# Optimization experiments

Hardware: AMD Instinct MI355X
Metric: run time of the kernel (lower is better)

Reference implementation:

```python
import jax, jax.numpy as jnp
import numpy as np

D_MODEL = 512
N_PAIRS = D_MODEL // 2
B, T = 8, 4096


def setup_inputs() -> dict:
    key = jax.random.key(0)
    ks = jax.random.split(key, 7)
    scale = 1.0 / np.sqrt(D_MODEL)
    return {
        "x_seq": jax.random.normal(ks[0], (B, T, D_MODEL), dtype=jnp.float32),
        "W_angle": jax.random.uniform(ks[1], (D_MODEL, N_PAIRS), jnp.float32, -scale, scale),
        "b_angle": jnp.zeros((N_PAIRS,), jnp.float32),
        "W_decay": jax.random.uniform(ks[2], (D_MODEL, 1), jnp.float32, -scale, scale),
        "b_decay": jnp.full((1,), 1.4, jnp.float32),
        "W_input": jax.random.uniform(ks[3], (D_MODEL, D_MODEL), jnp.float32, -scale, scale),
        "b_input": jax.random.uniform(ks[4], (D_MODEL,), jnp.float32, -scale, scale),
    }


def _givens_ssm(x_seq, W_angle, b_angle, W_decay, b_decay, W_input, b_input):
    Bb, Tt, D = x_seq.shape
    P = D // 2
    angles = jnp.einsum("btd,dp->btp", x_seq, W_angle) + b_angle          # [B,T,P]
    decays = jax.nn.sigmoid(jnp.einsum("btd,dk->btk", x_seq, W_decay) + b_decay)[..., 0]  # [B,T]
    inj = jnp.einsum("btd,de->bte", x_seq, W_input) + b_input              # [B,T,D]
    inj = inj.reshape(Bb, Tt, P, 2)

    # scan over time: h_t = decay_t * Rot(angles_t) h_{t-1} + inj_t, pairwise 2x2 rotations
    def step(h, inp):
        a, d, u = inp  # a:[B,P], d:[B], u:[B,P,2]
        c, s = jnp.cos(a), jnp.sin(a)
        he = c * h[..., 0] - s * h[..., 1]
        ho = s * h[..., 0] + c * h[..., 1]
        h_new = d[:, None, None] * jnp.stack([he, ho], axis=-1) + u
        return h_new, h_new

    h0 = jnp.zeros((Bb, P, 2), x_seq.dtype)
    xs = (jnp.swapaxes(angles, 0, 1), jnp.swapaxes(decays, 0, 1), jnp.swapaxes(inj, 0, 1))
    _, states = jax.lax.scan(step, h0, xs)  # [T,B,P,2]
    return jnp.swapaxes(states, 0, 1).reshape(Bb, Tt, D)


def reference(x_seq, W_angle, b_angle, W_decay, b_decay, W_input, b_input):
    return _givens_ssm(x_seq, W_angle, b_angle, W_decay, b_decay, W_input, b_input)
```

## Files before the change

kernel.cpp:

```cpp
#include <hip/hip_runtime.h>
#include <math.h>

typedef _Float16 half_t;
typedef __attribute__((ext_vector_type(8))) _Float16 half8;
typedef __attribute__((ext_vector_type(2))) _Float16 half2v;
typedef __attribute__((ext_vector_type(4))) float floatx4;

#define BATCH   8
#define SEQ     4096
#define DM      512
#define NP      256
#define M_TOT   32768
#define NTOT    768
#define CHUNKS  128
#define CHUNK_LEN 32

__device__ __forceinline__ void async_load16(const void* g, void* l) {
    __builtin_amdgcn_global_load_lds((const __attribute__((address_space(1))) void*)g,
                                     (__attribute__((address_space(3))) void*)l,
                                     16, 0, 0);
}

__global__ __launch_bounds__(256) void decay_convert(const float* __restrict__ X,
                                                     const float* __restrict__ Wd,
                                                     const float* __restrict__ bd,
                                                     float* __restrict__ dec,
                                                     half_t* __restrict__ Xh) {
    const int wave = threadIdx.x >> 6;
    const int lane = threadIdx.x & 63;
    const int row0 = blockIdx.x * 8 + wave * 2;
    const float4* x0 = (const float4*)(X + (size_t)row0 * DM);
    const float4* x1 = x0 + 128;
    const float4* wd = (const float4*)Wd;
    float4 a0 = x0[2 * lane], a1 = x0[2 * lane + 1];
    float4 b0 = x1[2 * lane], b1 = x1[2 * lane + 1];
    float4 w0 = wd[2 * lane], w1 = wd[2 * lane + 1];
    float s0 = a0.x * w0.x + a0.y * w0.y + a0.z * w0.z + a0.w * w0.w
             + a1.x * w1.x + a1.y * w1.y + a1.z * w1.z + a1.w * w1.w;
    float s1 = b0.x * w0.x + b0.y * w0.y + b0.z * w0.z + b0.w * w0.w
             + b1.x * w1.x + b1.y * w1.y + b1.z * w1.z + b1.w * w1.w;
    half8 h0 = {(half_t)a0.x, (half_t)a0.y, (half_t)a0.z, (half_t)a0.w,
                (half_t)a1.x, (half_t)a1.y, (half_t)a1.z, (half_t)a1.w};
    half8 h1 = {(half_t)b0.x, (half_t)b0.y, (half_t)b0.z, (half_t)b0.w,
                (half_t)b1.x, (half_t)b1.y, (half_t)b1.z, (half_t)b1.w};
    *(half8*)(Xh + (size_t)row0 * DM + lane * 8) = h0;
    *(half8*)(Xh + (size_t)(row0 + 1) * DM + lane * 8) = h1;
#pragma unroll
    for (int off = 32; off > 0; off >>= 1) {
        s0 += __shfl_down(s0, off, 64);
        s1 += __shfl_down(s1, off, 64);
    }
    if (lane == 0) {
        dec[row0]     = 1.0f / (1.0f + __expf(-(s0 + bd[0])));
        dec[row0 + 1] = 1.0f / (1.0f + __expf(-(s1 + bd[0])));
    }
}

__global__ __launch_bounds__(256) void wcat_transpose(const float* __restrict__ Wi,
                                                      const float* __restrict__ Wa,
                                                      half_t* __restrict__ Wt) {
    const int idx = blockIdx.x * 256 + threadIdx.x;
    const int n = idx >> 9;
    const int k = idx & 511;
    float v = (n < DM) ? Wi[(size_t)k * DM + n] : Wa[(size_t)k * NP + (n - DM)];
    Wt[idx] = (half_t)v;
}

__global__ __launch_bounds__(256) void gemm_fused(const half_t* __restrict__ Xh,
                                                  const half_t* __restrict__ Wt,
                                                  const float* __restrict__ bi,
                                                  const float* __restrict__ ba,
                                                  float* __restrict__ out,
                                                  half_t* __restrict__ angles) {
    __shared__ __align__(16) char As[8192];
    __shared__ __align__(16) char Bs[8192];

    const int bm   = blockIdx.x;
    const int bn   = blockIdx.y;
    const int tid  = threadIdx.x;
    const int wave = tid >> 6;
    const int lane = tid & 63;
    const int quad = lane >> 4;
    const int l16  = lane & 15;
    const int wrow = wave >> 1;
    const int wcol = wave & 1;

    floatx4 acc[4][4];
#pragma unroll
    for (int i = 0; i < 4; ++i)
#pragma unroll
        for (int j = 0; j < 4; ++j) acc[i][j] = (floatx4){0.f, 0.f, 0.f, 0.f};

    const int s0 = wave * 128 + lane;
    const int s1 = s0 + 64;
    const int r0 = s0 >> 2, kql0 = (s0 & 3) ^ ((r0 >> 1) & 3);
    const int r1 = s1 >> 2, kql1 = (s1 & 3) ^ ((r1 >> 1) & 3);
    const half_t* gA0 = Xh + (size_t)(bm * 128 + r0) * DM + kql0 * 8;
    const half_t* gA1 = Xh + (size_t)(bm * 128 + r1) * DM + kql1 * 8;
    const half_t* gB0 = Wt + (size_t)(bn * 128 + r0) * DM + kql0 * 8;
    const half_t* gB1 = Wt + (size_t)(bn * 128 + r1) * DM + kql1 * 8;
    char* lA0 = As + wave * 2048;
    char* lA1 = As + wave * 2048 + 1024;
    char* lB0 = Bs + wave * 2048;
    char* lB1 = Bs + wave * 2048 + 1024;

    for (int k0 = 0; k0 < DM; k0 += 32) {
        async_load16(gA0 + k0, lA0);
        async_load16(gA1 + k0, lA1);
        async_load16(gB0 + k0, lB0);
        async_load16(gB1 + k0, lB1);
        __syncthreads();

        half8 af[4], bf[4];
#pragma unroll
        for (int mt = 0; mt < 4; ++mt) {
            const int r = wrow * 64 + mt * 16 + l16;
            af[mt] = *(const half8*)(As + r * 64 + ((quad ^ ((r >> 1) & 3)) << 4));
        }
#pragma unroll
        for (int nt = 0; nt < 4; ++nt) {
            const int r = wcol * 64 + nt * 16 + l16;
            bf[nt] = *(const half8*)(Bs + r * 64 + ((quad ^ ((r >> 1) & 3)) << 4));
        }
#pragma unroll
        for (int mt = 0; mt < 4; ++mt)
#pragma unroll
            for (int nt = 0; nt < 4; ++nt)
                acc[mt][nt] = __builtin_amdgcn_mfma_f32_16x16x32_f16(af[mt], bf[nt],
                                                                     acc[mt][nt], 0, 0, 0);
        __syncthreads();
    }

    const int colbase = bn * 128 + wcol * 64;
#pragma unroll
    for (int nt = 0; nt < 4; ++nt) {
        const int col = colbase + nt * 16 + l16;
        const bool is_inj = col < DM;
        const float bias = is_inj ? bi[col] : ba[col - DM];
#pragma unroll
        for (int mt = 0; mt < 4; ++mt) {
            const int rowb = bm * 128 + wrow * 64 + mt * 16 + quad * 4;
#pragma unroll
            for (int r = 0; r < 4; ++r) {
                const float v = acc[mt][nt][r] + bias;
                const int row = rowb + r;
                if (is_inj) out[(size_t)row * DM + col] = v;
                else        angles[(size_t)row * NP + (col - DM)] = (half_t)v;
            }
        }
    }
}

__global__ __launch_bounds__(256) void scan_sum1(const half_t* __restrict__ angles,
                                                 const float* __restrict__ decays,
                                                 const float* __restrict__ inj,
                                                 float* __restrict__ thetaC,
                                                 float4* __restrict__ hend,
                                                 float* __restrict__ Dprod) {
    const int b   = blockIdx.x >> 6;
    const int sub = threadIdx.x >> 7;
    const int th  = threadIdx.x & 127;
    const int c   = (blockIdx.x & 63) * 2 + sub;
    const int p0  = th * 2;
    const int t0  = c * CHUNK_LEN;

    const half_t* ap = angles + (size_t)(b * SEQ + t0) * NP + p0;
    const float4* up = (const float4*)inj + (size_t)(b * SEQ + t0) * 128 + (p0 >> 1);
    const float*  dp = decays + b * SEQ + t0;

    half2v ab[2][8]; float4 ub[2][8]; float db[2][8];
#pragma unroll
    for (int j = 0; j < 8; ++j) {
        ab[0][j] = *(const half2v*)(ap + (size_t)j * NP);
        ub[0][j] = up[(size_t)j * 128];
        db[0][j] = dp[j];
    }

    float h0a = 0, h1a = 0, h0b = 0, h1b = 0, tha = 0, thb = 0, dc = 1.0f;
#pragma unroll
    for (int g = 0; g < 4; ++g) {
        const int cur = g & 1, nxt = cur ^ 1;
        if (g < 3) {
#pragma unroll
            for (int j = 0; j < 8; ++j) {
                const int t = (g + 1) * 8 + j;
                ab[nxt][j] = *(const half2v*)(ap + (size_t)t * NP);
                ub[nxt][j] = up[(size_t)t * 128];
                db[nxt][j] = dp[t];
            }
        }
#pragma unroll
        for (int j = 0; j < 8; ++j) {
            float a0 = (float)ab[cur][j][0], a1 = (float)ab[cur][j][1];
            float4 u = ub[cur][j];
            float d  = db[cur][j];
            float s0, c0, s1, c1;
            __sincosf(a0, &s0, &c0);
            __sincosf(a1, &s1, &c1);
            float n0a = fmaf(d, c0 * h0a - s0 * h1a, u.x);
            float n1a = fmaf(d, s0 * h0a + c0 * h1a, u.y);
            float n0b = fmaf(d, c1 * h0b - s1 * h1b, u.z);
            float n1b = fmaf(d, s1 * h0b + c1 * h1b, u.w);
            h0a = n0a; h1a = n1a; h0b = n0b; h1b = n1b;
            tha += a0; thb += a1; dc *= d;
        }
    }
    const size_t cbase = (size_t)(b * CHUNKS + c) * NP + p0;
    *(float2*)(thetaC + cbase) = make_float2(tha, thb);
    hend[cbase >> 1] = make_float4(h0a, h1a, h0b, h1b);
    if (th == 0) Dprod[b * CHUNKS + c] = dc;
}

__global__ __launch_bounds__(128) void scan_chunks(const float* __restrict__ thetaC,
                                                   const float4* __restrict__ hend,
                                                   const float* __restrict__ Dprod,
                                                   float4* __restrict__ hentry) {
    const int b  = blockIdx.x;
    const int p0 = threadIdx.x * 2;
    const float2* tp = (const float2*)thetaC + (size_t)b * CHUNKS * 128 + (p0 >> 1);
    const float4* hp = hend + (size_t)b * CHUNKS * 128 + (p0 >> 1);
    float4*       ep = hentry + (size_t)b * CHUNKS * 128 + (p0 >> 1);
    const float*  Dp = Dprod + b * CHUNKS;

    float2 tb[2][4]; float4 hb[2][4]; float Db[2][4];
#pragma unroll
    for (int j = 0; j < 4; ++j) {
        tb[0][j] = tp[(size_t)j * 128];
        hb[0][j] = hp[(size_t)j * 128];
        Db[0][j] = Dp[j];
    }

    float h0a = 0, h1a = 0, h0b = 0, h1b = 0;
#pragma unroll
    for (int g = 0; g < 32; ++g) {
        const int cur = g & 1, nxt = cur ^ 1;
        if (g < 31) {
#pragma unroll
            for (int j = 0; j < 4; ++j) {
                const int c = (g + 1) * 4 + j;
                tb[nxt][j] = tp[(size_t)c * 128];
                hb[nxt][j] = hp[(size_t)c * 128];
                Db[nxt][j] = Dp[c];
            }
        }
#pragma unroll
        for (int j = 0; j < 4; ++j) {
            const int c = g * 4 + j;
            ep[(size_t)c * 128] = make_float4(h0a, h1a, h0b, h1b);
            float2 th2 = tb[cur][j];
            float4 he  = hb[cur][j];
            float D    = Db[cur][j];
            float s0, c0, s1, c1;
            __sincosf(th2.x, &s0, &c0);
            __sincosf(th2.y, &s1, &c1);
            float n0a = fmaf(D, c0 * h0a - s0 * h1a, he.x);
            float n1a = fmaf(D, s0 * h0a + c0 * h1a, he.y);
            float n0b = fmaf(D, c1 * h0b - s1 * h1b, he.z);
            float n1b = fmaf(D, s1 * h0b + c1 * h1b, he.w);
            h0a = n0a; h1a = n1a; h0b = n0b; h1b = n1b;
        }
    }
}

__global__ __launch_bounds__(256) void scan_final(const half_t* __restrict__ angles,
                                                  const float* __restrict__ decays,
                                                  const float4* __restrict__ hentry,
                                                  float* __restrict__ out) {
    const int b   = blockIdx.x >> 6;
    const int sub = threadIdx.x >> 7;
    const int th  = threadIdx.x & 127;
    const int c   = (blockIdx.x & 63) * 2 + sub;
    const int p0  = th * 2;
    const int t0  = c * CHUNK_LEN;

    const half_t* ap = angles + (size_t)(b * SEQ + t0) * NP + p0;
    float4*       op = (float4*)out + (size_t)(b * SEQ + t0) * 128 + (p0 >> 1);
    const float*  dp = decays + b * SEQ + t0;

    float4 v = hentry[(size_t)(b * CHUNKS + c) * 128 + (p0 >> 1)];
    float h0a = v.x, h1a = v.y, h0b = v.z, h1b = v.w;

    half2v ab[2][8]; float4 ub[2][8]; float db[2][8];
#pragma unroll
    for (int j = 0; j < 8; ++j) {
        ab[0][j] = *(const half2v*)(ap + (size_t)j * NP);
        ub[0][j] = op[(size_t)j * 128];
        db[0][j] = dp[j];
    }

#pragma unroll
    for (int g = 0; g < 4; ++g) {
        const int cur = g & 1, nxt = cur ^ 1;
        if (g < 3) {
#pragma unroll
            for (int j = 0; j < 8; ++j) {
                const int t = (g + 1) * 8 + j;
                ab[nxt][j] = *(const half2v*)(ap + (size_t)t * NP);
                ub[nxt][j] = op[(size_t)t * 128];
                db[nxt][j] = dp[t];
            }
        }
#pragma unroll
        for (int j = 0; j < 8; ++j) {
            const int t = g * 8 + j;
            float a0 = (float)ab[cur][j][0], a1 = (float)ab[cur][j][1];
            float4 u = ub[cur][j];
            float d  = db[cur][j];
            float s0, c0, s1, c1;
            __sincosf(a0, &s0, &c0);
            __sincosf(a1, &s1, &c1);
            float n0a = fmaf(d, c0 * h0a - s0 * h1a, u.x);
            float n1a = fmaf(d, s0 * h0a + c0 * h1a, u.y);
            float n0b = fmaf(d, c1 * h0b - s1 * h1b, u.z);
            float n1b = fmaf(d, s1 * h0b + c1 * h1b, u.w);
            h0a = n0a; h1a = n1a; h0b = n0b; h1b = n1b;
            op[(size_t)t * 128] = make_float4(h0a, h1a, h0b, h1b);
        }
    }
}

extern "C" void kernel_launch(void* const* d_in, const int* in_sizes, int n_in,
                              void* d_out, int out_size, void* d_ws, size_t ws_size,
                              hipStream_t stream) {
    const float* x  = (const float*)d_in[0];
    const float* Wa = (const float*)d_in[1];
    const float* ba = (const float*)d_in[2];
    const float* Wd = (const float*)d_in[3];
    const float* bd = (const float*)d_in[4];
    const float* Wi = (const float*)d_in[5];
    const float* bi = (const float*)d_in[6];
    float* out = (float*)d_out;

    char* ws = (char*)d_ws;
    half_t* x_h     = (half_t*)(ws);
    float*  thetaC  = (float*)(ws);
    float4* hend    = (float4*)(ws + 1048576);
    float*  Dprod   = (float*)(ws + 3145728);
    float4* hentry  = (float4*)(ws + 3149824);
    half_t* angles  = (half_t*)(ws + 33554432);
    float*  decays  = (float*)(ws + 50331648);
    half_t* Wcat_t  = (half_t*)(ws + 50462720);

    decay_convert<<<M_TOT / 8, 256, 0, stream>>>(x, Wd, bd, decays, x_h);
    wcat_transpose<<<(NTOT * DM) / 256, 256, 0, stream>>>(Wi, Wa, Wcat_t);
    gemm_fused<<<dim3(M_TOT / 128, NTOT / 128), 256, 0, stream>>>(x_h, Wcat_t, bi, ba, out, angles);

    scan_sum1<<<BATCH * CHUNKS / 2, 256, 0, stream>>>(angles, decays, out, thetaC, hend, Dprod);
    scan_chunks<<<BATCH, 128, 0, stream>>>(thetaC, hend, Dprod, hentry);
    scan_final<<<BATCH * CHUNKS / 2, 256, 0, stream>>>(angles, decays, hentry, out);
}
```

Baseline: 218.1 us.

## Parallelize chunk-carry scan with block-level Hillis-Steele scan and halve chunk length

Replaces the serial 128-step carry propagation (only 8 blocks of 128 threads) with a parallel Hillis-Steele prefix scan over 256 chunks in shared memory, one block per (batch, pair-of-pairs). Chunk length drops from 32 to 16, doubling the chunk count so the first and last scan passes launch twice as many blocks. The aim is to remove the long serial latency chain of the middle pass, which badly underfills the GPU. In exchange the scan does log-depth extra work with many __syncthreads and more sincos calls. Workspace offsets are moved to fit the larger intermediate buffers.

Result: no change. 220.5 us (+1.1%).

```diff
diff --git a/kernel.cpp b/kernel.cpp
--- a/kernel.cpp
+++ b/kernel.cpp
@@ -12,8 +12,8 @@
 #define NP      256
 #define M_TOT   32768
 #define NTOT    768
-#define CHUNKS  128
-#define CHUNK_LEN 32
+#define CHUNKS  256
+#define CHUNK_LEN 16
 
 __device__ __forceinline__ void async_load16(const void* g, void* l) {
     __builtin_amdgcn_global_load_lds((const __attribute__((address_space(1))) void*)g,
@@ -157,10 +157,10 @@
                                                  float* __restrict__ thetaC,
                                                  float4* __restrict__ hend,
                                                  float* __restrict__ Dprod) {
-    const int b   = blockIdx.x >> 6;
+    const int b   = blockIdx.x >> 7;
     const int sub = threadIdx.x >> 7;
     const int th  = threadIdx.x & 127;
-    const int c   = (blockIdx.x & 63) * 2 + sub;
+    const int c   = (blockIdx.x & 127) * 2 + sub;
     const int p0  = th * 2;
     const int t0  = c * CHUNK_LEN;
 
@@ -178,9 +178,9 @@
 
     float h0a = 0, h1a = 0, h0b = 0, h1b = 0, tha = 0, thb = 0, dc = 1.0f;
 #pragma unroll
-    for (int g = 0; g < 4; ++g) {
+    for (int g = 0; g < 2; ++g) {
         const int cur = g & 1, nxt = cur ^ 1;
-        if (g < 3) {
+        if (g < 1) {
 #pragma unroll
             for (int j = 0; j < 8; ++j) {
                 const int t = (g + 1) * 8 + j;
@@ -211,65 +211,58 @@
     if (th == 0) Dprod[b * CHUNKS + c] = dc;
 }
 
-__global__ __launch_bounds__(128) void scan_chunks(const float* __restrict__ thetaC,
+__global__ __launch_bounds__(256) void scan_chunks(const float* __restrict__ thetaC,
                                                    const float4* __restrict__ hend,
                                                    const float* __restrict__ Dprod,
                                                    float4* __restrict__ hentry) {
-    const int b  = blockIdx.x;
-    const int p0 = threadIdx.x * 2;
-    const float2* tp = (const float2*)thetaC + (size_t)b * CHUNKS * 128 + (p0 >> 1);
-    const float4* hp = hend + (size_t)b * CHUNKS * 128 + (p0 >> 1);
-    float4*       ep = hentry + (size_t)b * CHUNKS * 128 + (p0 >> 1);
-    const float*  Dp = Dprod + b * CHUNKS;
-
-    float2 tb[2][4]; float4 hb[2][4]; float Db[2][4];
-#pragma unroll
-    for (int j = 0; j < 4; ++j) {
-        tb[0][j] = tp[(size_t)j * 128];
-        hb[0][j] = hp[(size_t)j * 128];
-        Db[0][j] = Dp[j];
-    }
-
-    float h0a = 0, h1a = 0, h0b = 0, h1b = 0;
-#pragma unroll
-    for (int g = 0; g < 32; ++g) {
-        const int cur = g & 1, nxt = cur ^ 1;
-        if (g < 31) {
-#pragma unroll
-            for (int j = 0; j < 4; ++j) {
-                const int c = (g + 1) * 4 + j;
-                tb[nxt][j] = tp[(size_t)c * 128];
-                hb[nxt][j] = hp[(size_t)c * 128];
-                Db[nxt][j] = Dp[c];
-            }
-        }
-#pragma unroll
-        for (int j = 0; j < 4; ++j) {
-            const int c = g * 4 + j;
-            ep[(size_t)c * 128] = make_float4(h0a, h1a, h0b, h1b);
-            float2 th2 = tb[cur][j];
-            float4 he  = hb[cur][j];
-            float D    = Db[cur][j];
+    const int b  = blockIdx.x >> 7;
+    const int pp = blockIdx.x & 127;
+    const int c  = threadIdx.x;
+
+    __shared__ float  sTa[256], sTb[256], sD[256];
+    __shared__ float4 sV[256];
+
+    const size_t idx = (size_t)(b * CHUNKS + c);
+    const float2 th2 = *(const float2*)(thetaC + idx * NP + pp * 2);
+    float4 v = hend[idx * 128 + pp];
+    float  D = Dprod[idx];
+    float tha = th2.x, thb = th2.y;
+
+    sTa[c] = tha; sTb[c] = thb; sD[c] = D; sV[c] = v;
+
+#pragma unroll
+    for (int o = 1; o < 256; o <<= 1) {
+        __syncthreads();
+        float lta = 0.f, ltb = 0.f, lD = 0.f;
+        float4 lv = make_float4(0.f, 0.f, 0.f, 0.f);
+        const bool has = (c >= o);
+        if (has) { lta = sTa[c - o]; ltb = sTb[c - o]; lD = sD[c - o]; lv = sV[c - o]; }
+        __syncthreads();
+        if (has) {
             float s0, c0, s1, c1;
-            __sincosf(th2.x, &s0, &c0);
-            __sincosf(th2.y, &s1, &c1);
-            float n0a = fmaf(D, c0 * h0a - s0 * h1a, he.x);
-            float n1a = fmaf(D, s0 * h0a + c0 * h1a, he.y);
-            float n0b = fmaf(D, c1 * h0b - s1 * h1b, he.z);
-            float n1b = fmaf(D, s1 * h0b + c1 * h1b, he.w);
-            h0a = n0a; h1a = n1a; h0b = n0b; h1b = n1b;
-        }
-    }
+            __sincosf(tha, &s0, &c0);
+            __sincosf(thb, &s1, &c1);
+            v.x = fmaf(D, c0 * lv.x - s0 * lv.y, v.x);
+            v.y = fmaf(D, s0 * lv.x + c0 * lv.y, v.y);
+            v.z = fmaf(D, c1 * lv.z - s1 * lv.w, v.z);
+            v.w = fmaf(D, s1 * lv.z + c1 * lv.w, v.w);
+            tha += lta; thb += ltb; D *= lD;
+            sTa[c] = tha; sTb[c] = thb; sD[c] = D; sV[c] = v;
+        }
+    }
+    __syncthreads();
+    const float4 e = (c == 0) ? make_float4(0.f, 0.f, 0.f, 0.f) : sV[c - 1];
+    hentry[idx * 128 + pp] = e;
 }
 
 __global__ __launch_bounds__(256) void scan_final(const half_t* __restrict__ angles,
                                                   const float* __restrict__ decays,
                                                   const float4* __restrict__ hentry,
                                                   float* __restrict__ out) {
-    const int b   = blockIdx.x >> 6;
+    const int b   = blockIdx.x >> 7;
     const int sub = threadIdx.x >> 7;
     const int th  = threadIdx.x & 127;
-    const int c   = (blockIdx.x & 63) * 2 + sub;
+    const int c   = (blockIdx.x & 127) * 2 + sub;
     const int p0  = th * 2;
     const int t0  = c * CHUNK_LEN;
 
@@ -289,9 +282,9 @@
     }
 
 #pragma unroll
-    for (int g = 0; g < 4; ++g) {
+    for (int g = 0; g < 2; ++g) {
         const int cur = g & 1, nxt = cur ^ 1;
-        if (g < 3) {
+        if (g < 1) {
 #pragma unroll
             for (int j = 0; j < 8; ++j) {
                 const int t = (g + 1) * 8 + j;
@@ -334,9 +327,9 @@
     char* ws = (char*)d_ws;
     half_t* x_h     = (half_t*)(ws);
     float*  thetaC  = (float*)(ws);
-    float4* hend    = (float4*)(ws + 1048576);
-    float*  Dprod   = (float*)(ws + 3145728);
-    float4* hentry  = (float4*)(ws + 3149824);
+    float4* hend    = (float4*)(ws + 2097152);
+    float*  Dprod   = (float*)(ws + 6291456);
+    float4* hentry  = (float4*)(ws + 6299648);
     half_t* angles  = (half_t*)(ws + 33554432);
     float*  decays  = (float*)(ws + 50331648);
     half_t* Wcat_t  = (half_t*)(ws + 50462720);
@@ -346,6 +339,6 @@
     gemm_fused<<<dim3(M_TOT / 128, NTOT / 128), 256, 0, stream>>>(x_h, Wcat_t, bi, ba, out, angles);
 
     scan_sum1<<<BATCH * CHUNKS / 2, 256, 0, stream>>>(angles, decays, out, thetaC, hend, Dprod);
-    scan_chunks<<<BATCH, 128, 0, stream>>>(thetaC, hend, Dprod, hentry);
+    scan_chunks<<<BATCH * 128, 256, 0, stream>>>(thetaC, hend, Dprod, hentry);
     scan_final<<<BATCH * CHUNKS / 2, 256, 0, stream>>>(angles, decays, hentry, out);
 }
```
